# Kernel optimization log

Hardware: AMD Instinct MI355X
Metric: run time of the kernel (lower is better)

## Reference

```python
import jax, jax.numpy as jnp
import numpy as np

N, C, R = 8192, 512, 8
DK = C // R  # 64

def setup_inputs() -> dict:
    key = jax.random.key(0)
    k1, k2, kq, kk, kv = jax.random.split(key, 5)
    s = 0.05
    return {
        "im1": jax.random.normal(k1, (N, C), jnp.float32),
        "im2": jax.random.normal(k2, (N, C), jnp.float32),
        "Wq": jax.random.normal(kq, (C, DK), jnp.float32) * s,
        "Wk": jax.random.normal(kk, (C, DK), jnp.float32) * s,
        "Wv": jax.random.normal(kv, (C, C), jnp.float32) * s,
    }

def reference(im1, im2, Wq, Wk, Wv):
    # shared projections (weights stored as [in, out]; torch Linear is x @ W.T)
    im1_q = im1 @ Wq  # [N, DK]
    im1_k = im1 @ Wk  # [N, DK]
    im1_v = im1 @ Wv  # [N, C]
    im2_q = im2 @ Wq
    im2_k = im2 @ Wk
    im2_v = im2 @ Wv
    # cross attention (no scaling in original)
    im1_attn = jax.nn.softmax(im2_q @ im1_k.T, axis=-1)  # [N, N]
    im2_attn = jax.nn.softmax(im1_q @ im2_k.T, axis=-1)  # [N, N]
    im1_out = im1_attn @ im1_v + im1
    im2_out = im2_attn @ im2_v + im2
    return im1_out, im2_out
```

## Files before the change

### kernel.cpp

```cpp
#include <hip/hip_runtime.h>

#define NN 8192
#define CC 512
#define DKK 64

typedef float f32x4 __attribute__((ext_vector_type(4)));
typedef float f32x16 __attribute__((ext_vector_type(16)));
typedef _Float16 f16x8 __attribute__((ext_vector_type(8)));
typedef _Float16 f16x4 __attribute__((ext_vector_type(4)));

__device__ __forceinline__ f32x4 mfma16(f16x8 a, f16x8 b, f32x4 c) {
    return __builtin_amdgcn_mfma_f32_16x16x32_f16(a, b, c, 0, 0, 0);
}
__device__ __forceinline__ f32x16 mfma32(f16x8 a, f16x8 b, f32x16 c) {
    return __builtin_amdgcn_mfma_f32_32x32x16_f16(a, b, c, 0, 0, 0);
}
__device__ __forceinline__ f16x8 scl8(f16x8 v, float f) {
    _Float16 h = (_Float16)f;
    f16x8 r;
#pragma unroll
    for (int i = 0; i < 8; i++) r[i] = v[i] * h;
    return r;
}

__global__ void wtrans_all_kernel(const float* __restrict__ Wq, const float* __restrict__ Wk,
                                  const float* __restrict__ Wv,
                                  _Float16* __restrict__ Wqt, _Float16* __restrict__ Wkt,
                                  _Float16* __restrict__ Wvf) {
    int idx = blockIdx.x * 256 + threadIdx.x;
    if (idx < 32768) {
        int n = idx >> 9, k = idx & 511;
        Wqt[idx] = (_Float16)Wq[k * 64 + n];
    } else if (idx < 65536) {
        int j = idx - 32768;
        int n = j >> 9, k = j & 511;
        Wkt[j] = (_Float16)Wk[k * 64 + n];
    } else {
        int j = idx - 65536;
        int k16 = j & 15, c = (j >> 4) & 511, ks = j >> 13;
        Wvf[j] = (_Float16)Wv[(size_t)(16 * ks + k16) * 512 + c];
    }
}

__global__ __launch_bounds__(256) void proj_qk2_kernel(
    const float* __restrict__ im1, const float* __restrict__ im2,
    const _Float16* __restrict__ Wqt, const _Float16* __restrict__ Wkt,
    _Float16* __restrict__ Q1, _Float16* __restrict__ Kf1,
    _Float16* __restrict__ Q2, _Float16* __restrict__ Kf2)
{
    const float* X = blockIdx.y ? im2 : im1;
    _Float16* Q = blockIdx.y ? Q2 : Q1;
    _Float16* Kf = blockIdx.y ? Kf2 : Kf1;

    __shared__ __align__(16) _Float16 Wlds[128 * 512];

    const int tid = threadIdx.x;
    const int lane = tid & 63, wave = tid >> 6;
    const int n16 = lane & 15, quad = lane >> 4;

#pragma unroll
    for (int i = 0; i < 32; i++) {
        const int idx = tid + 256 * i;
        const int row = idx >> 6, ch = idx & 63;
        const _Float16* src = (row < 64) ? (Wqt + (size_t)row * 512 + ch * 8)
                                         : (Wkt + (size_t)(row - 64) * 512 + ch * 8);
        *(f16x8*)&Wlds[row * 512 + ((ch ^ (row & 7)) * 8)] = *(const f16x8*)src;
    }
    __syncthreads();

    const int arow = blockIdx.x * 64 + wave * 16 + n16;
    f32x4 acc[8];
#pragma unroll
    for (int i = 0; i < 8; i++) acc[i] = (f32x4){0.f, 0.f, 0.f, 0.f};

    const float* xbase = X + (size_t)arow * 512 + quad * 8;
    for (int kk = 0; kk < 16; kk++) {
        f32x4 xa = *(const f32x4*)(xbase + kk * 32);
        f32x4 xb = *(const f32x4*)(xbase + kk * 32 + 4);
        f16x8 afrag;
#pragma unroll
        for (int j = 0; j < 4; j++) { afrag[j] = (_Float16)xa[j]; afrag[4 + j] = (_Float16)xb[j]; }
#pragma unroll
        for (int t = 0; t < 8; t++) {
            const int row = t * 16 + n16;
            f16x8 bfr = *(const f16x8*)&Wlds[row * 512 + (((4 * kk + quad) ^ (row & 7)) * 8)];
            acc[t] = mfma16(afrag, bfr, acc[t]);
        }
    }
    const int rbase = blockIdx.x * 64 + wave * 16 + quad * 4;
#pragma unroll
    for (int t = 0; t < 4; t++)
#pragma unroll
        for (int r = 0; r < 4; r++) {
            Q[(size_t)(rbase + r) * 64 + t * 16 + n16] = (_Float16)acc[t][r];
            Kf[((size_t)(blockIdx.x * 4 + t) * 64 + (wave * 16 + quad * 4 + r)) * 16 + n16] =
                (_Float16)acc[4 + t][r];
        }
}

__global__ __launch_bounds__(256) void proj_vt_kernel(
    const float* __restrict__ im1, const float* __restrict__ im2,
    const _Float16* __restrict__ Wvf,
    _Float16* __restrict__ Vf1, _Float16* __restrict__ Vf2)
{
    const float* X = blockIdx.y ? im2 : im1;
    _Float16* Vf = blockIdx.y ? Vf2 : Vf1;
    const int n0 = blockIdx.x * 32;
    const int tid = threadIdx.x;
    const int lane = tid & 63, wave = tid >> 6;
    const int l31 = lane & 31, lhi = lane >> 5;

    __shared__ __align__(16) _Float16 Xlds[32 * 512];

#pragma unroll
    for (int i = 0; i < 8; i++) {
        const int n = tid >> 3;
        const int chunk = (tid & 7) + 8 * i;
        const float* xp = X + (size_t)(n0 + n) * CC + chunk * 8;
        f32x4 x0 = *(const f32x4*)xp;
        f32x4 x1 = *(const f32x4*)(xp + 4);
        f16x8 d;
#pragma unroll
        for (int j = 0; j < 4; j++) { d[j] = (_Float16)x0[j]; d[4 + j] = (_Float16)x1[j]; }
        *(f16x8*)&Xlds[n * 512 + ((chunk ^ (n & 7)) * 8)] = d;
    }
    __syncthreads();

    f32x16 acc[4];
#pragma unroll
    for (int t = 0; t < 4; t++)
#pragma unroll
        for (int r = 0; r < 16; r++) acc[t][r] = 0.f;

    for (int ks = 0; ks < 32; ks++) {
        f16x8 xb = *(const f16x8*)&Xlds[l31 * 512 + (((2 * ks + lhi) ^ (l31 & 7)) * 8)];
#pragma unroll
        for (int ct = 0; ct < 4; ct++) {
            const _Float16* wp = Wvf + ((size_t)ks * 512 + 128 * wave + 32 * ct + l31) * 16 + 8 * lhi;
            acc[ct] = mfma32(*(const f16x8*)wp, xb, acc[ct]);
        }
    }
    const int tile = n0 >> 6;
    const int ksbase = (n0 & 32) >> 4;
#pragma unroll
    for (int ct = 0; ct < 4; ct++)
#pragma unroll
        for (int r = 0; r < 16; r++) {
            const int c = 128 * wave + 32 * ct + (r & 3) + 8 * (r >> 2) + 4 * lhi;
            const int ks = ksbase + (l31 >> 4);
            Vf[((size_t)(tile * 4 + ks) * 512 + c) * 16 + (l31 & 15)] = (_Float16)acc[ct][r];
        }
}

__global__ __launch_bounds__(512, 2) void flash5_kernel(
    const _Float16* __restrict__ Q1, const _Float16* __restrict__ Kf1,
    const _Float16* __restrict__ Q2, const _Float16* __restrict__ Kf2,
    const _Float16* __restrict__ Vf1, const _Float16* __restrict__ Vf2,
    const float* __restrict__ im1, const float* __restrict__ im2,
    float* __restrict__ out)
{
    const int img = blockIdx.y;
    const _Float16* Q = img ? Q1 : Q2;
    const _Float16* Kf = img ? Kf2 : Kf1;
    const _Float16* Vf = img ? Vf2 : Vf1;
    const float* res = img ? im2 : im1;
    float* o = out + (size_t)img * NN * CC;

    __shared__ __align__(16) char smem[64 * 516 * 4];
    __shared__ float mPart[2][2][2][64];
    __shared__ float mF[2][2][64], lF[2][2][64];

    const int tid = threadIdx.x;
    const int lane = tid & 63, wave = tid >> 6;
    const int l31 = lane & 31, lhi = lane >> 5;
    const int g = wave >> 2, wg = wave & 3;
    const int b = wg & 1, a = wg >> 1;
    const int qbase = blockIdx.x * 64;

    _Float16* Pbase = (_Float16*)smem;

    f16x8 qf[4];
    {
        const _Float16* qp = Q + (size_t)(qbase + 32 * b + l31) * DKK + 8 * lhi;
#pragma unroll
        for (int k = 0; k < 4; k++) qf[k] = *(const f16x8*)(qp + 16 * k);
    }

    f32x16 acc[8];
#pragma unroll
    for (int t = 0; t < 8; t++)
#pragma unroll
        for (int r = 0; r < 16; r++) acc[t][r] = 0.f;
    float ma_run = -3e38f, l_run = 0.f;
    float mg_run[2] = {-3e38f, -3e38f};

    auto do_qk = [&](int s) {
        const int t = 2 * s + g;
        const int pbuf = s & 1;
        _Float16* Pg = Pbase + (pbuf * 2 + g) * 4096;
        f32x16 sA;
#pragma unroll
        for (int r = 0; r < 16; r++) sA[r] = 0.f;
#pragma unroll
        for (int k = 0; k < 4; k++) {
            f16x8 kf = *(const f16x8*)(Kf + ((size_t)(t * 4 + k) * 64 + 32 * a + l31) * 16 + 8 * lhi);
            sA = mfma32(kf, qf[k], sA);
        }
        float mx = -3e38f;
#pragma unroll
        for (int r = 0; r < 16; r++) mx = fmaxf(mx, sA[r]);
        mx = fmaxf(mx, __shfl_xor(mx, 32));
        const float manew = fmaxf(ma_run, mx);
        if (lane < 32) mPart[pbuf][g][a][32 * b + lane] = manew;
        float ls = 0.f;
#pragma unroll
        for (int r = 0; r < 16; r++) {
            float p = __expf(sA[r] - manew);
            ls += p;
            sA[r] = p;
        }
        ls += __shfl_xor(ls, 32);
        l_run = l_run * __expf(ma_run - manew) + ls;
        ma_run = manew;
        const int q = 32 * b + l31;
#pragma unroll
        for (int gg = 0; gg < 4; gg++) {
            f16x4 p4;
#pragma unroll
            for (int u = 0; u < 4; u++) p4[u] = (_Float16)sA[gg * 4 + u];
            *(f16x4*)&Pg[((4 * a + gg) * 64 + q) * 8 + 4 * lhi] = p4;
        }
    };

    do_qk(0);
    __syncthreads();

    for (int s = 0; s < 64; s++) {
        const int t = 2 * s + g;
        const int pbuf = s & 1;
        _Float16* Pg = Pbase + (pbuf * 2 + g) * 4096;

        f16x8 va01[8];
#pragma unroll
        for (int k = 0; k < 2; k++)
#pragma unroll
            for (int ct = 0; ct < 4; ct++)
                va01[k * 4 + ct] = *(const f16x8*)(Vf +
                    ((size_t)(t * 4 + k) * 512 + 128 * wg + 32 * ct + l31) * 16 + 8 * lhi);

        if (s < 63) do_qk(s + 1);

        float al[2], f0[2], f1[2];
#pragma unroll
        for (int qt = 0; qt < 2; qt++) {
            const int q = 32 * qt + l31;
            const float m0 = mPart[pbuf][g][0][q];
            const float m1 = mPart[pbuf][g][1][q];
            const float mgn = fmaxf(mg_run[qt], fmaxf(m0, m1));
            al[qt] = __expf(mg_run[qt] - mgn);
            f0[qt] = __expf(m0 - mgn);
            f1[qt] = __expf(m1 - mgn);
            mg_run[qt] = mgn;
        }
        if (!__all((al[0] == 1.f) & (al[1] == 1.f))) {
#pragma unroll
            for (int ct = 0; ct < 4; ct++)
#pragma unroll
                for (int r = 0; r < 16; r++) {
                    acc[ct * 2 + 0][r] *= al[0];
                    acc[ct * 2 + 1][r] *= al[1];
                }
        }
        const bool noscale =
            __all((f0[0] == 1.f) & (f1[0] == 1.f) & (f0[1] == 1.f) & (f1[1] == 1.f));
#pragma unroll
        for (int k = 0; k < 4; k++) {
            f16x8 pb0 = *(const f16x8*)&Pg[((2 * k + lhi) * 64 + l31) * 8];
            f16x8 pb1 = *(const f16x8*)&Pg[((2 * k + lhi) * 64 + 32 + l31) * 8];
            if (!noscale) {
                pb0 = scl8(pb0, k < 2 ? f0[0] : f1[0]);
                pb1 = scl8(pb1, k < 2 ? f0[1] : f1[1]);
            }
#pragma unroll
            for (int ct = 0; ct < 4; ct++) {
                f16x8 va;
                if (k < 2) va = va01[k * 4 + ct];
                else va = *(const f16x8*)(Vf +
                    ((size_t)(t * 4 + k) * 512 + 128 * wg + 32 * ct + l31) * 16 + 8 * lhi);
                acc[ct * 2 + 0] = mfma32(va, pb0, acc[ct * 2 + 0]);
                acc[ct * 2 + 1] = mfma32(va, pb1, acc[ct * 2 + 1]);
            }
        }
        __syncthreads();
    }

    if (lane < 32) {
        mF[g][a][32 * b + lane] = ma_run;
        lF[g][a][32 * b + lane] = l_run;
    }
    __syncthreads();

    float fac[2];
#pragma unroll
    for (int qt = 0; qt < 2; qt++) {
        const int q = 32 * qt + l31;
        const float m00 = mF[0][0][q], m01 = mF[0][1][q];
        const float m10 = mF[1][0][q], m11 = mF[1][1][q];
        const float M = fmaxf(fmaxf(m00, m01), fmaxf(m10, m11));
        const float den = lF[0][0][q] * __expf(m00 - M) + lF[0][1][q] * __expf(m01 - M) +
                          lF[1][0][q] * __expf(m10 - M) + lF[1][1][q] * __expf(m11 - M);
        fac[qt] = __expf(mg_run[qt] - M) / den;
    }

    float* Olds = (float*)smem;
    if (g == 0) {
#pragma unroll
        for (int ct = 0; ct < 4; ct++)
#pragma unroll
            for (int qt = 0; qt < 2; qt++)
#pragma unroll
                for (int r = 0; r < 16; r++) {
                    const int c = 128 * wg + 32 * ct + (r & 3) + 8 * (r >> 2) + 4 * lhi;
                    Olds[(32 * qt + l31) * 516 + c] = acc[ct * 2 + qt][r] * fac[qt];
                }
    }
    __syncthreads();
    if (g == 1) {
#pragma unroll
        for (int ct = 0; ct < 4; ct++)
#pragma unroll
            for (int qt = 0; qt < 2; qt++)
#pragma unroll
                for (int r = 0; r < 16; r++) {
                    const int c = 128 * wg + 32 * ct + (r & 3) + 8 * (r >> 2) + 4 * lhi;
                    Olds[(32 * qt + l31) * 516 + c] += acc[ct * 2 + qt][r] * fac[qt];
                }
    }
    __syncthreads();

    {
        const int q = tid >> 3;
        const size_t grow = (size_t)(qbase + q);
#pragma unroll
        for (int i = 0; i < 16; i++) {
            const int cw = ((tid & 7) + 8 * i) * 4;
            f32x4 v = *(const f32x4*)&Olds[q * 516 + cw];
            f32x4 rr = *(const f32x4*)(res + grow * CC + cw);
            v += rr;
            *(f32x4*)(o + grow * CC + cw) = v;
        }
    }
}

extern "C" void kernel_launch(void* const* d_in, const int* in_sizes, int n_in,
                              void* d_out, int out_size, void* d_ws, size_t ws_size,
                              hipStream_t stream) {
    const float* im1 = (const float*)d_in[0];
    const float* im2 = (const float*)d_in[1];
    const float* Wq  = (const float*)d_in[2];
    const float* Wk  = (const float*)d_in[3];
    const float* Wv  = (const float*)d_in[4];
    float* out = (float*)d_out;

    _Float16* w = (_Float16*)d_ws;
    _Float16* Wqt = w;
    _Float16* Wkt = Wqt + 64 * 512;
    _Float16* Wvf = Wkt + 64 * 512;
    _Float16* Q1  = Wvf + 512 * 512;
    _Float16* Kf1 = Q1 + NN * DKK;
    _Float16* Q2  = Kf1 + NN * DKK;
    _Float16* Kf2 = Q2 + NN * DKK;
    _Float16* Vf1 = Kf2 + NN * DKK;
    _Float16* Vf2 = Vf1 + (size_t)CC * NN;

    wtrans_all_kernel<<<1280, 256, 0, stream>>>(Wq, Wk, Wv, Wqt, Wkt, Wvf);
    proj_qk2_kernel<<<dim3(128, 2), 256, 0, stream>>>(im1, im2, Wqt, Wkt, Q1, Kf1, Q2, Kf2);
    proj_vt_kernel<<<dim3(256, 2), 256, 0, stream>>>(im1, im2, Wvf, Vf1, Vf2);
    flash5_kernel<<<dim3(128, 2), 512, 0, stream>>>(Q1, Kf1, Q2, Kf2, Vf1, Vf2, im1, im2, out);
}
```

Baseline: 422.0 us.

## Split attention output channels across two blocks per query tile

The attention kernel now launches a third grid dimension that splits the 512 output channels into two halves. Each block computes only 256 channels, recomputing the QK scores and softmax statistics for its query tile. This halves the accumulator registers and shrinks the output staging buffer in shared memory, and the launch bound now allows 4 blocks per SM. The aim is to double the block count and raise occupancy to hide latency better, at the cost of doing the QK and softmax work twice.

```diff
diff --git a/kernel.cpp b/kernel.cpp
--- a/kernel.cpp
+++ b/kernel.cpp
@@ -152,7 +152,7 @@
         }
 }
 
-__global__ __launch_bounds__(512, 2) void flash5_kernel(
+__global__ __launch_bounds__(512, 4) void flash6_kernel(
     const _Float16* __restrict__ Q1, const _Float16* __restrict__ Kf1,
     const _Float16* __restrict__ Q2, const _Float16* __restrict__ Kf2,
     const _Float16* __restrict__ Vf1, const _Float16* __restrict__ Vf2,
@@ -160,13 +160,14 @@
     float* __restrict__ out)
 {
     const int img = blockIdx.y;
+    const int ch = blockIdx.z;
     const _Float16* Q = img ? Q1 : Q2;
     const _Float16* Kf = img ? Kf2 : Kf1;
     const _Float16* Vf = img ? Vf2 : Vf1;
     const float* res = img ? im2 : im1;
     float* o = out + (size_t)img * NN * CC;
 
-    __shared__ __align__(16) char smem[64 * 516 * 4];
+    __shared__ __align__(16) char smem[64 * 132 * 4];
     __shared__ float mPart[2][2][2][64];
     __shared__ float mF[2][2][64], lF[2][2][64];
 
@@ -176,6 +177,7 @@
     const int g = wave >> 2, wg = wave & 3;
     const int b = wg & 1, a = wg >> 1;
     const int qbase = blockIdx.x * 64;
+    const int cbase = 256 * ch + 64 * wg;
 
     _Float16* Pbase = (_Float16*)smem;
 
@@ -186,9 +188,9 @@
         for (int k = 0; k < 4; k++) qf[k] = *(const f16x8*)(qp + 16 * k);
     }
 
-    f32x16 acc[8];
-#pragma unroll
-    for (int t = 0; t < 8; t++)
+    f32x16 acc[4];
+#pragma unroll
+    for (int t = 0; t < 4; t++)
 #pragma unroll
         for (int r = 0; r < 16; r++) acc[t][r] = 0.f;
     float ma_run = -3e38f, l_run = 0.f;
@@ -240,13 +242,13 @@
         const int pbuf = s & 1;
         _Float16* Pg = Pbase + (pbuf * 2 + g) * 4096;
 
-        f16x8 va01[8];
+        f16x8 va01[4];
 #pragma unroll
         for (int k = 0; k < 2; k++)
 #pragma unroll
-            for (int ct = 0; ct < 4; ct++)
-                va01[k * 4 + ct] = *(const f16x8*)(Vf +
-                    ((size_t)(t * 4 + k) * 512 + 128 * wg + 32 * ct + l31) * 16 + 8 * lhi);
+            for (int ct = 0; ct < 2; ct++)
+                va01[k * 2 + ct] = *(const f16x8*)(Vf +
+                    ((size_t)(t * 4 + k) * 512 + cbase + 32 * ct + l31) * 16 + 8 * lhi);
 
         if (s < 63) do_qk(s + 1);
 
@@ -264,7 +266,7 @@
         }
         if (!__all((al[0] == 1.f) & (al[1] == 1.f))) {
 #pragma unroll
-            for (int ct = 0; ct < 4; ct++)
+            for (int ct = 0; ct < 2; ct++)
 #pragma unroll
                 for (int r = 0; r < 16; r++) {
                     acc[ct * 2 + 0][r] *= al[0];
@@ -282,11 +284,11 @@
                 pb1 = scl8(pb1, k < 2 ? f0[1] : f1[1]);
             }
 #pragma unroll
-            for (int ct = 0; ct < 4; ct++) {
+            for (int ct = 0; ct < 2; ct++) {
                 f16x8 va;
-                if (k < 2) va = va01[k * 4 + ct];
+                if (k < 2) va = va01[k * 2 + ct];
                 else va = *(const f16x8*)(Vf +
-                    ((size_t)(t * 4 + k) * 512 + 128 * wg + 32 * ct + l31) * 16 + 8 * lhi);
+                    ((size_t)(t * 4 + k) * 512 + cbase + 32 * ct + l31) * 16 + 8 * lhi);
                 acc[ct * 2 + 0] = mfma32(va, pb0, acc[ct * 2 + 0]);
                 acc[ct * 2 + 1] = mfma32(va, pb1, acc[ct * 2 + 1]);
             }
@@ -313,41 +315,47 @@
     }
 
     float* Olds = (float*)smem;
-    if (g == 0) {
-#pragma unroll
-        for (int ct = 0; ct < 4; ct++)
-#pragma unroll
-            for (int qt = 0; qt < 2; qt++)
-#pragma unroll
-                for (int r = 0; r < 16; r++) {
-                    const int c = 128 * wg + 32 * ct + (r & 3) + 8 * (r >> 2) + 4 * lhi;
-                    Olds[(32 * qt + l31) * 516 + c] = acc[ct * 2 + qt][r] * fac[qt];
-                }
-    }
-    __syncthreads();
-    if (g == 1) {
-#pragma unroll
-        for (int ct = 0; ct < 4; ct++)
-#pragma unroll
-            for (int qt = 0; qt < 2; qt++)
-#pragma unroll
-                for (int r = 0; r < 16; r++) {
-                    const int c = 128 * wg + 32 * ct + (r & 3) + 8 * (r >> 2) + 4 * lhi;
-                    Olds[(32 * qt + l31) * 516 + c] += acc[ct * 2 + qt][r] * fac[qt];
-                }
-    }
-    __syncthreads();
-
-    {
-        const int q = tid >> 3;
-        const size_t grow = (size_t)(qbase + q);
-#pragma unroll
-        for (int i = 0; i < 16; i++) {
-            const int cw = ((tid & 7) + 8 * i) * 4;
-            f32x4 v = *(const f32x4*)&Olds[q * 516 + cw];
-            f32x4 rr = *(const f32x4*)(res + grow * CC + cw);
-            v += rr;
-            *(f32x4*)(o + grow * CC + cw) = v;
+#pragma unroll
+    for (int rr = 0; rr < 2; rr++) {
+        const bool mine = ((wg >> 1) == rr);
+        const int cloc = 64 * (wg & 1);
+        __syncthreads();
+        if (mine && g == 0) {
+#pragma unroll
+            for (int ct = 0; ct < 2; ct++)
+#pragma unroll
+                for (int qt = 0; qt < 2; qt++)
+#pragma unroll
+                    for (int r = 0; r < 16; r++) {
+                        const int c = cloc + 32 * ct + (r & 3) + 8 * (r >> 2) + 4 * lhi;
+                        Olds[(32 * qt + l31) * 132 + c] = acc[ct * 2 + qt][r] * fac[qt];
+                    }
+        }
+        __syncthreads();
+        if (mine && g == 1) {
+#pragma unroll
+            for (int ct = 0; ct < 2; ct++)
+#pragma unroll
+                for (int qt = 0; qt < 2; qt++)
+#pragma unroll
+                    for (int r = 0; r < 16; r++) {
+                        const int c = cloc + 32 * ct + (r & 3) + 8 * (r >> 2) + 4 * lhi;
+                        Olds[(32 * qt + l31) * 132 + c] += acc[ct * 2 + qt][r] * fac[qt];
+                    }
+        }
+        __syncthreads();
+        {
+            const int q = tid >> 3;
+            const size_t grow = (size_t)(qbase + q);
+            const int cg = 256 * ch + 128 * rr;
+#pragma unroll
+            for (int i = 0; i < 4; i++) {
+                const int cw = ((tid & 7) + 8 * i) * 4;
+                f32x4 v = *(const f32x4*)&Olds[q * 132 + cw];
+                f32x4 rrv = *(const f32x4*)(res + grow * CC + cg + cw);
+                v += rrv;
+                *(f32x4*)(o + grow * CC + cg + cw) = v;
+            }
         }
     }
 }
@@ -376,5 +384,5 @@
     wtrans_all_kernel<<<1280, 256, 0, stream>>>(Wq, Wk, Wv, Wqt, Wkt, Wvf);
     proj_qk2_kernel<<<dim3(128, 2), 256, 0, stream>>>(im1, im2, Wqt, Wkt, Q1, Kf1, Q2, Kf2);
     proj_vt_kernel<<<dim3(256, 2), 256, 0, stream>>>(im1, im2, Wvf, Vf1, Vf2);
-    flash5_kernel<<<dim3(128, 2), 512, 0, stream>>>(Q1, Kf1, Q2, Kf2, Vf1, Vf2, im1, im2, out);
-}
+    flash6_kernel<<<dim3(128, 2, 2), 512, 0, stream>>>(Q1, Kf1, Q2, Kf2, Vf1, Vf2, im1, im2, out);
+}
```

Measured after the change: 477.7 us. 1.13x slower.
